# Optimization experiments

Measured on AMD Instinct MI355X. Metric: run time of the kernel, lower is better.

The kernel has to match this reference:

```python
import jax, jax.numpy as jnp
import numpy as np

N_FEATURES = 512
BATCH = 32768
MISS_RATE = 0.5


def setup_inputs() -> dict:
    key = jax.random.key(0)
    kx, km, kmu, kw = jax.random.split(key, 4)
    x = jax.random.normal(kx, (BATCH, N_FEATURES), dtype=jnp.float32)
    miss = jax.random.bernoulli(km, MISS_RATE, (BATCH, N_FEATURES))
    x = jnp.where(miss, jnp.nan, x)  # NaNs encode missing entries
    mu = jax.random.normal(kmu, (N_FEATURES,), dtype=jnp.float32)
    # xavier_uniform with gain=0.5: bound = 0.5*sqrt(6/(fan_in+fan_out))
    bound = 0.5 * np.sqrt(6.0 / (2 * N_FEATURES))
    W = jax.random.uniform(kw, (N_FEATURES, N_FEATURES), dtype=jnp.float32,
                           minval=-bound, maxval=bound)
    return {"x": x, "mu": mu, "W": W, "depth": 10}


def reference(x, mu, W, depth):
    miss = jnp.isnan(x)                     # [B, F] bool
    obs = (~miss).astype(x.dtype)           # ~mask in the torch code
    x0 = jnp.where(miss, 0.0, x)            # nan_to_num
    h0 = x0 - obs * mu                      # initial h; also the skip value

    def step(h, _):
        # Linear (tied W, no bias) -> mask -> residual skip to h0
        h = obs * (h @ W.T) + h0
        return h, None

    h, _ = jax.lax.scan(step, h0, None, length=depth)
    return h
```

## Files before the change

### kernel.cpp

```cpp
#include <hip/hip_runtime.h>
#include <hip/hip_bf16.h>
#include <stdint.h>

#define NF 512
#define DEPTH 10
#define RPB 64
#define NBLK 512
#define THREADS 512

typedef __attribute__((ext_vector_type(8))) short s16x8;
typedef __attribute__((ext_vector_type(4))) float f32x4;

__device__ __forceinline__ unsigned short f2b(float f) {
    unsigned int u = __float_as_uint(f);
    u += 0x7FFFu + ((u >> 16) & 1u);
    return (unsigned short)(u >> 16);
}
__device__ __forceinline__ float b2f(unsigned short b) {
    return __uint_as_float(((unsigned int)b) << 16);
}

__global__ void prep_wpack(const float* __restrict__ W, unsigned short* __restrict__ Wp) {
    int t = blockIdx.x * blockDim.x + threadIdx.x;
    int l  = t & 63;
    int a  = (t >> 6) & 3;
    int ks = (t >> 8) & 15;
    int wc = t >> 12;
    int row = wc * 64 + a * 16 + (l & 15);
    int kb  = ks * 32 + (l >> 4) * 8;
    const float* src = W + (size_t)row * NF + kb;
    float4 va = *(const float4*)src;
    float4 vb = *(const float4*)(src + 4);
    union { s16x8 v; unsigned short u[8]; } o;
    o.u[0] = f2b(va.x); o.u[1] = f2b(va.y); o.u[2] = f2b(va.z); o.u[3] = f2b(va.w);
    o.u[4] = f2b(vb.x); o.u[5] = f2b(vb.y); o.u[6] = f2b(vb.z); o.u[7] = f2b(vb.w);
    *(s16x8*)(Wp + (size_t)t * 8) = o.v;
}

__device__ __forceinline__ unsigned short enc(float x, float mu) {
    if (x != x) return (unsigned short)0x8000u;
    unsigned short v = f2b(x - mu);
    return (v == 0x8000u) ? (unsigned short)0 : v;
}
__global__ void prep_h0(const float4* __restrict__ x4, const float4* __restrict__ mu4,
                        ushort4* __restrict__ h4) {
    int i = blockIdx.x * blockDim.x + threadIdx.x;
    float4 xv = x4[i];
    float4 m  = mu4[i & 127];
    ushort4 o;
    o.x = enc(xv.x, m.x); o.y = enc(xv.y, m.y);
    o.z = enc(xv.z, m.z); o.w = enc(xv.w, m.w);
    h4[i] = o;
}

__global__ void __launch_bounds__(THREADS, 2)
nm_fused(const unsigned short* __restrict__ Wp,
         const unsigned short* __restrict__ h0,
         float* __restrict__ out)
{
    __shared__ __align__(16) unsigned char hl[131072];

    const int tid  = threadIdx.x;
    const int lane = tid & 63;
    const int wc   = tid >> 6;
    const int l15  = lane & 15;
    const int g    = lane >> 4;
    const int row0 = blockIdx.x * RPB;

#pragma unroll
    for (int i = 0; i < 8; ++i) {
        int id  = tid + i * THREADS;
        int row = id >> 6, q = id & 63;
        s16x8 v = *(const s16x8*)(h0 + (size_t)(row0 + row) * NF + q * 8);
        *(s16x8*)(hl + q * 1024 + row * 16) = v;
    }

    const unsigned short* wq = Wp + ((size_t)(wc * 4096) + lane) * 8;
#define WLOAD(KS, A) (*(const s16x8*)(wq + (size_t)((KS) * 256 + (A) * 64) * 8))

    const int r16 = l15 << 4;
    const int gk  = g << 10;
#define HLOAD(CB, KS, MB) (*(const s16x8*)(hl + (CB) + (KS) * 4096 + gk + (MB) * 256 + r16))

    const int colb = wc * 64 + g * 4;
    const unsigned short* h0p = h0 + (size_t)(row0 + l15) * NF + colb;
    float* outp = out + (size_t)(row0 + l15) * NF + colb;

    ushort4 h0r[4][4];
#pragma unroll
    for (int mb = 0; mb < 4; ++mb)
#pragma unroll
        for (int a = 0; a < 4; ++a)
            h0r[mb][a] = *(const ushort4*)(h0p + (size_t)(mb * 16) * NF + a * 16);

    const int wb  = (g >> 1) << 10;
    const int hb8 = (g & 1) << 3;

    __syncthreads();

    for (int d = 0; d < DEPTH; ++d) {
        const int curb = (d & 1) << 16;
        const int nxtb = curb ^ 65536;
        f32x4 acc[4][4] = {};

#pragma unroll 4
        for (int ks = 0; ks < 16; ++ks) {
            s16x8 wf0 = WLOAD(ks, 0), wf1 = WLOAD(ks, 1);
            s16x8 wf2 = WLOAD(ks, 2), wf3 = WLOAD(ks, 3);
            s16x8 hf0 = HLOAD(curb, ks, 0), hf1 = HLOAD(curb, ks, 1);
            s16x8 hf2 = HLOAD(curb, ks, 2), hf3 = HLOAD(curb, ks, 3);
            acc[0][0] = __builtin_amdgcn_mfma_f32_16x16x32_bf16(wf0, hf0, acc[0][0], 0, 0, 0);
            acc[0][1] = __builtin_amdgcn_mfma_f32_16x16x32_bf16(wf1, hf0, acc[0][1], 0, 0, 0);
            acc[0][2] = __builtin_amdgcn_mfma_f32_16x16x32_bf16(wf2, hf0, acc[0][2], 0, 0, 0);
            acc[0][3] = __builtin_amdgcn_mfma_f32_16x16x32_bf16(wf3, hf0, acc[0][3], 0, 0, 0);
            acc[1][0] = __builtin_amdgcn_mfma_f32_16x16x32_bf16(wf0, hf1, acc[1][0], 0, 0, 0);
            acc[1][1] = __builtin_amdgcn_mfma_f32_16x16x32_bf16(wf1, hf1, acc[1][1], 0, 0, 0);
            acc[1][2] = __builtin_amdgcn_mfma_f32_16x16x32_bf16(wf2, hf1, acc[1][2], 0, 0, 0);
            acc[1][3] = __builtin_amdgcn_mfma_f32_16x16x32_bf16(wf3, hf1, acc[1][3], 0, 0, 0);
            acc[2][0] = __builtin_amdgcn_mfma_f32_16x16x32_bf16(wf0, hf2, acc[2][0], 0, 0, 0);
            acc[2][1] = __builtin_amdgcn_mfma_f32_16x16x32_bf16(wf1, hf2, acc[2][1], 0, 0, 0);
            acc[2][2] = __builtin_amdgcn_mfma_f32_16x16x32_bf16(wf2, hf2, acc[2][2], 0, 0, 0);
            acc[2][3] = __builtin_amdgcn_mfma_f32_16x16x32_bf16(wf3, hf2, acc[2][3], 0, 0, 0);
            acc[3][0] = __builtin_amdgcn_mfma_f32_16x16x32_bf16(wf0, hf3, acc[3][0], 0, 0, 0);
            acc[3][1] = __builtin_amdgcn_mfma_f32_16x16x32_bf16(wf1, hf3, acc[3][1], 0, 0, 0);
            acc[3][2] = __builtin_amdgcn_mfma_f32_16x16x32_bf16(wf2, hf3, acc[3][2], 0, 0, 0);
            acc[3][3] = __builtin_amdgcn_mfma_f32_16x16x32_bf16(wf3, hf3, acc[3][3], 0, 0, 0);
        }

        if (d == DEPTH - 1) {
#pragma unroll
            for (int mb = 0; mb < 4; ++mb) {
#pragma unroll
                for (int a = 0; a < 4; ++a) {
                    ushort4 hb = h0r[mb][a];
                    float4 o;
                    o.x = (hb.x == 0x8000u) ? 0.f : acc[mb][a][0] + b2f(hb.x);
                    o.y = (hb.y == 0x8000u) ? 0.f : acc[mb][a][1] + b2f(hb.y);
                    o.z = (hb.z == 0x8000u) ? 0.f : acc[mb][a][2] + b2f(hb.z);
                    o.w = (hb.w == 0x8000u) ? 0.f : acc[mb][a][3] + b2f(hb.w);
                    *(float4*)(outp + (size_t)(mb * 16) * NF + a * 16) = o;
                }
            }
        } else {
#pragma unroll
            for (int mb = 0; mb < 4; ++mb) {
#pragma unroll
                for (int a = 0; a < 4; ++a) {
                    ushort4 hb = h0r[mb][a];
                    ushort4 o;
                    o.x = (hb.x == 0x8000u) ? (unsigned short)0 : f2b(acc[mb][a][0] + b2f(hb.x));
                    o.y = (hb.y == 0x8000u) ? (unsigned short)0 : f2b(acc[mb][a][1] + b2f(hb.y));
                    o.z = (hb.z == 0x8000u) ? (unsigned short)0 : f2b(acc[mb][a][2] + b2f(hb.z));
                    o.w = (hb.w == 0x8000u) ? (unsigned short)0 : f2b(acc[mb][a][3] + b2f(hb.w));
                    *(ushort4*)(hl + nxtb + wc * 8192 + a * 2048 + wb + mb * 256 + r16 + hb8) = o;
                }
            }
            __syncthreads();
        }
    }
#undef HLOAD
#undef WLOAD
}

extern "C" void kernel_launch(void* const* d_in, const int* in_sizes, int n_in,
                              void* d_out, int out_size, void* d_ws, size_t ws_size,
                              hipStream_t stream) {
    const float* x  = (const float*)d_in[0];
    const float* mu = (const float*)d_in[1];
    const float* W  = (const float*)d_in[2];
    float* out = (float*)d_out;

    char* ws = (char*)d_ws;
    unsigned short* Wp = (unsigned short*)ws;
    unsigned short* h0 = (unsigned short*)(ws + (1u << 19));

    prep_wpack<<<128,   256, 0, stream>>>(W, Wp);
    prep_h0   <<<16384, 256, 0, stream>>>((const float4*)x, (const float4*)mu, (ushort4*)h0);
    nm_fused  <<<NBLK, THREADS, 0, stream>>>(Wp, h0, out);
}
```

Measured before the change: 199.2 us.

## Double rows per block to 128, single-buffer LDS, reload skip values from global

Each block now processes 128 rows instead of 64, so every W fragment loaded from global feeds twice as many MFMAs and the total W traffic across blocks is halved. The double-buffered LDS h tile becomes a single 128 KB buffer, with an extra barrier between the MMA loop and the write-back. The per-thread register cache of h0 skip values is removed and they are re-read from global memory each depth step to free registers for the larger 8x4 accumulator array. The cost is fewer blocks (256, roughly one per CU with low occupancy), an extra sync per iteration, and repeated global reads of h0.

```diff
diff --git a/kernel.cpp b/kernel.cpp
--- a/kernel.cpp
+++ b/kernel.cpp
@@ -4,8 +4,8 @@
 
 #define NF 512
 #define DEPTH 10
-#define RPB 64
-#define NBLK 512
+#define RPB 128
+#define NBLK 256
 #define THREADS 512
 
 typedef __attribute__((ext_vector_type(8))) short s16x8;
@@ -68,71 +68,52 @@
     const int row0 = blockIdx.x * RPB;
 
 #pragma unroll
-    for (int i = 0; i < 8; ++i) {
+    for (int i = 0; i < 16; ++i) {
         int id  = tid + i * THREADS;
         int row = id >> 6, q = id & 63;
         s16x8 v = *(const s16x8*)(h0 + (size_t)(row0 + row) * NF + q * 8);
-        *(s16x8*)(hl + q * 1024 + row * 16) = v;
+        *(s16x8*)(hl + q * 2048 + row * 16) = v;
     }
 
     const unsigned short* wq = Wp + ((size_t)(wc * 4096) + lane) * 8;
 #define WLOAD(KS, A) (*(const s16x8*)(wq + (size_t)((KS) * 256 + (A) * 64) * 8))
 
-    const int r16 = l15 << 4;
-    const int gk  = g << 10;
-#define HLOAD(CB, KS, MB) (*(const s16x8*)(hl + (CB) + (KS) * 4096 + gk + (MB) * 256 + r16))
+    const int hbase = g * 2048 + l15 * 16;
+#define HLOAD(KS, MB) (*(const s16x8*)(hl + (KS) * 8192 + (MB) * 256 + hbase))
 
     const int colb = wc * 64 + g * 4;
     const unsigned short* h0p = h0 + (size_t)(row0 + l15) * NF + colb;
     float* outp = out + (size_t)(row0 + l15) * NF + colb;
 
-    ushort4 h0r[4][4];
-#pragma unroll
-    for (int mb = 0; mb < 4; ++mb)
-#pragma unroll
-        for (int a = 0; a < 4; ++a)
-            h0r[mb][a] = *(const ushort4*)(h0p + (size_t)(mb * 16) * NF + a * 16);
-
-    const int wb  = (g >> 1) << 10;
-    const int hb8 = (g & 1) << 3;
+    const int wb  = (g >> 1) * 2048 + (g & 1) * 8 + l15 * 16;
 
     __syncthreads();
 
     for (int d = 0; d < DEPTH; ++d) {
-        const int curb = (d & 1) << 16;
-        const int nxtb = curb ^ 65536;
-        f32x4 acc[4][4] = {};
+        f32x4 acc[8][4] = {};
 
-#pragma unroll 4
+#pragma unroll 2
         for (int ks = 0; ks < 16; ++ks) {
             s16x8 wf0 = WLOAD(ks, 0), wf1 = WLOAD(ks, 1);
             s16x8 wf2 = WLOAD(ks, 2), wf3 = WLOAD(ks, 3);
-            s16x8 hf0 = HLOAD(curb, ks, 0), hf1 = HLOAD(curb, ks, 1);
-            s16x8 hf2 = HLOAD(curb, ks, 2), hf3 = HLOAD(curb, ks, 3);
-            acc[0][0] = __builtin_amdgcn_mfma_f32_16x16x32_bf16(wf0, hf0, acc[0][0], 0, 0, 0);
-            acc[0][1] = __builtin_amdgcn_mfma_f32_16x16x32_bf16(wf1, hf0, acc[0][1], 0, 0, 0);
-            acc[0][2] = __builtin_amdgcn_mfma_f32_16x16x32_bf16(wf2, hf0, acc[0][2], 0, 0, 0);
-            acc[0][3] = __builtin_amdgcn_mfma_f32_16x16x32_bf16(wf3, hf0, acc[0][3], 0, 0, 0);
-            acc[1][0] = __builtin_amdgcn_mfma_f32_16x16x32_bf16(wf0, hf1, acc[1][0], 0, 0, 0);
-            acc[1][1] = __builtin_amdgcn_mfma_f32_16x16x32_bf16(wf1, hf1, acc[1][1], 0, 0, 0);
-            acc[1][2] = __builtin_amdgcn_mfma_f32_16x16x32_bf16(wf2, hf1, acc[1][2], 0, 0, 0);
-            acc[1][3] = __builtin_amdgcn_mfma_f32_16x16x32_bf16(wf3, hf1, acc[1][3], 0, 0, 0);
-            acc[2][0] = __builtin_amdgcn_mfma_f32_16x16x32_bf16(wf0, hf2, acc[2][0], 0, 0, 0);
-            acc[2][1] = __builtin_amdgcn_mfma_f32_16x16x32_bf16(wf1, hf2, acc[2][1], 0, 0, 0);
-            acc[2][2] = __builtin_amdgcn_mfma_f32_16x16x32_bf16(wf2, hf2, acc[2][2], 0, 0, 0);
-            acc[2][3] = __builtin_amdgcn_mfma_f32_16x16x32_bf16(wf3, hf2, acc[2][3], 0, 0, 0);
-            acc[3][0] = __builtin_amdgcn_mfma_f32_16x16x32_bf16(wf0, hf3, acc[3][0], 0, 0, 0);
-            acc[3][1] = __builtin_amdgcn_mfma_f32_16x16x32_bf16(wf1, hf3, acc[3][1], 0, 0, 0);
-            acc[3][2] = __builtin_amdgcn_mfma_f32_16x16x32_bf16(wf2, hf3, acc[3][2], 0, 0, 0);
-            acc[3][3] = __builtin_amdgcn_mfma_f32_16x16x32_bf16(wf3, hf3, acc[3][3], 0, 0, 0);
+#pragma unroll
+            for (int mb = 0; mb < 8; ++mb) {
+                s16x8 hf = HLOAD(ks, mb);
+                acc[mb][0] = __builtin_amdgcn_mfma_f32_16x16x32_bf16(wf0, hf, acc[mb][0], 0, 0, 0);
+                acc[mb][1] = __builtin_amdgcn_mfma_f32_16x16x32_bf16(wf1, hf, acc[mb][1], 0, 0, 0);
+                acc[mb][2] = __builtin_amdgcn_mfma_f32_16x16x32_bf16(wf2, hf, acc[mb][2], 0, 0, 0);
+                acc[mb][3] = __builtin_amdgcn_mfma_f32_16x16x32_bf16(wf3, hf, acc[mb][3], 0, 0, 0);
+            }
         }
+
+        __syncthreads();
 
         if (d == DEPTH - 1) {
 #pragma unroll
-            for (int mb = 0; mb < 4; ++mb) {
+            for (int mb = 0; mb < 8; ++mb) {
 #pragma unroll
                 for (int a = 0; a < 4; ++a) {
-                    ushort4 hb = h0r[mb][a];
+                    ushort4 hb = *(const ushort4*)(h0p + (size_t)(mb * 16) * NF + a * 16);
                     float4 o;
                     o.x = (hb.x == 0x8000u) ? 0.f : acc[mb][a][0] + b2f(hb.x);
                     o.y = (hb.y == 0x8000u) ? 0.f : acc[mb][a][1] + b2f(hb.y);
@@ -143,16 +124,16 @@
             }
         } else {
 #pragma unroll
-            for (int mb = 0; mb < 4; ++mb) {
+            for (int mb = 0; mb < 8; ++mb) {
 #pragma unroll
                 for (int a = 0; a < 4; ++a) {
-                    ushort4 hb = h0r[mb][a];
+                    ushort4 hb = *(const ushort4*)(h0p + (size_t)(mb * 16) * NF + a * 16);
                     ushort4 o;
                     o.x = (hb.x == 0x8000u) ? (unsigned short)0 : f2b(acc[mb][a][0] + b2f(hb.x));
                     o.y = (hb.y == 0x8000u) ? (unsigned short)0 : f2b(acc[mb][a][1] + b2f(hb.y));
                     o.z = (hb.z == 0x8000u) ? (unsigned short)0 : f2b(acc[mb][a][2] + b2f(hb.z));
                     o.w = (hb.w == 0x8000u) ? (unsigned short)0 : f2b(acc[mb][a][3] + b2f(hb.w));
-                    *(ushort4*)(hl + nxtb + wc * 8192 + a * 2048 + wb + mb * 256 + r16 + hb8) = o;
+                    *(ushort4*)(hl + (wc * 8 + a * 2) * 2048 + mb * 256 + wb) = o;
                 }
             }
             __syncthreads();
```

New measurement: 244.2 us. 22.6% more time.
